# Kernel optimization log

Hardware: AMD Instinct MI355X
Metric: run time of the kernel (lower is better)

## Reference

```python
import jax, jax.numpy as jnp
import numpy as np
from jax import lax


def extract_patches(x, kh, kw, sh, sw):
    # x: [B,H,W,C] -> [B,oh,ow,kh,kw,C], same element order as tf.image.extract_patches
    B, H, W, C = x.shape
    oh = (H - kh) // sh + 1
    ow = (W - kw) // sw + 1
    rows = jnp.arange(oh)[:, None] * sh + jnp.arange(kh)[None, :]  # [oh,kh]
    cols = jnp.arange(ow)[:, None] * sw + jnp.arange(kw)[None, :]  # [ow,kw]
    p = x[:, rows]            # [B,oh,kh,W,C]
    p = p[:, :, :, cols]      # [B,oh,kh,ow,kw,C]
    return jnp.transpose(p, (0, 1, 3, 2, 4, 5))  # [B,oh,ow,kh,kw,C]


def fastgrnn(x, W, U, bg, bu, zeta, nu):
    # FastGRNN: z=sigmoid(Wx+Uh+bg); c=tanh(Wx+Uh+bu); h'=z*h+(sig(zeta)*(1-z)+sig(nu))*c
    # x: [N,T,D] -> final hidden [N,H]
    wx = jnp.einsum('ntd,dh->nth', x, W)  # precompute input projection
    z_gate = jax.nn.sigmoid(zeta)
    n_gate = jax.nn.sigmoid(nu)

    def step(h, wx_t):
        pre = wx_t + h @ U
        z = jax.nn.sigmoid(pre + bg)
        c = jnp.tanh(pre + bu)
        h_new = z * h + (z_gate * (1.0 - z) + n_gate) * c
        return h_new, None

    h0 = jnp.zeros((x.shape[0], W.shape[1]), x.dtype)
    hT, _ = lax.scan(step, h0, jnp.swapaxes(wx, 0, 1))  # scan over T
    return hT


def rnnpool_forward(inputs, W1, U1, bg1, bu1, zeta1, nu1,
                    W2, U2, bg2, bu2, zeta2, nu2, kh, kw, sh, sw):
    B, H, Wd, C = inputs.shape
    oh = (H - kh) // sh + 1
    ow = (Wd - kw) // sw + 1
    patches = extract_patches(inputs, kh, kw, sh, sw)          # [B,oh,ow,kh,kw,C]
    N = B * oh * ow
    p = patches.reshape(N, kh, kw, C)

    u = W1.shape[1]
    # row-wise: rnn1 scans along cols within each row
    x = p.reshape(N * kh, kw, C)
    h = fastgrnn(x, W1, U1, bg1, bu1, zeta1, nu1).reshape(N, kh, u)
    o21 = fastgrnn(h, W2, U2, bg2, bu2, zeta2, nu2)
    o22 = fastgrnn(h[:, ::-1, :], W2, U2, bg2, bu2, zeta2, nu2)

    # col-wise: transpose patch, rnn1 scans along rows within each col
    xc = jnp.transpose(p, (0, 2, 1, 3)).reshape(N * kw, kh, C)
    hc = fastgrnn(xc, W1, U1, bg1, bu1, zeta1, nu1).reshape(N, kw, u)
    o23 = fastgrnn(hc, W2, U2, bg2, bu2, zeta2, nu2)
    o24 = fastgrnn(hc[:, ::-1, :], W2, U2, bg2, bu2, zeta2, nu2)

    out = jnp.concatenate([o21, o22, o23, o24], axis=1)        # [N, 4*hOut]
    return out.reshape(B, oh, ow, -1)


def setup_inputs() -> dict:
    key = jax.random.key(0)
    ks = jax.random.split(key, 9)
    C, u, hout = 16, 8, 16  # in-channels, rnn1 hidden, rnn2 hidden (out_channel//4)
    s = 0.1
    inp = {
        'inputs': jax.random.normal(ks[0], (32, 112, 112, C), jnp.float32),
        'W1': jax.random.normal(ks[1], (C, u), jnp.float32) * s,
        'U1': jax.random.normal(ks[2], (u, u), jnp.float32) * s,
        'bg1': jnp.ones((u,), jnp.float32),
        'bu1': jnp.ones((u,), jnp.float32),
        'zeta1': jnp.float32(100.0),
        'nu1': jnp.float32(-100.0),
        'W2': jax.random.normal(ks[3], (u, hout), jnp.float32) * s,
        'U2': jax.random.normal(ks[4], (hout, hout), jnp.float32) * s,
        'bg2': jnp.ones((hout,), jnp.float32),
        'bu2': jnp.ones((hout,), jnp.float32),
        'zeta2': jnp.float32(100.0),
        'nu2': jnp.float32(-100.0),
        'kh': 8, 'kw': 8, 'sh': 4, 'sw': 4,
    }
    return inp


def reference(inputs, W1, U1, bg1, bu1, zeta1, nu1,
              W2, U2, bg2, bu2, zeta2, nu2, kh, kw, sh, sw):
    return rnnpool_forward(inputs, W1, U1, bg1, bu1, zeta1, nu1,
                           W2, U2, bg2, bu2, zeta2, nu2, kh, kw, sh, sw)
```

## Files before the change

kernel.cpp:

```cpp
#include <hip/hip_runtime.h>

#define PPB 4

typedef float v2f __attribute__((ext_vector_type(2)));

__device__ __forceinline__ float frcp(float x) { return __builtin_amdgcn_rcpf(x); }

__device__ __forceinline__ v2f vfma2(v2f a, v2f b, v2f c) {
#if __has_builtin(__builtin_amdgcn_pk_fma_f32)
  return __builtin_amdgcn_pk_fma_f32(a, b, c);
#elif __has_builtin(__builtin_elementwise_fma)
  return __builtin_elementwise_fma(a, b, c);
#else
  v2f d; d.x = fmaf(a.x, b.x, c.x); d.y = fmaf(a.y, b.y, c.y); return d;
#endif
}
__device__ __forceinline__ v2f vmul2(v2f a, v2f b) {
#if __has_builtin(__builtin_amdgcn_pk_mul_f32)
  return __builtin_amdgcn_pk_mul_f32(a, b);
#else
  return a * b;
#endif
}
__device__ __forceinline__ v2f vadd2(v2f a, v2f b) {
#if __has_builtin(__builtin_amdgcn_pk_add_f32)
  return __builtin_amdgcn_pk_add_f32(a, b);
#else
  return a + b;
#endif
}
__device__ __forceinline__ v2f bc(float x) { v2f p; p.x = x; p.y = x; return p; }

__device__ __forceinline__ v2f gate2(v2f pre, v2f h, v2f bgB, v2f KB, v2f nzgB,
                                     v2f AB, bool first) {
  v2f a = vadd2(pre, bgB);
  v2f s; s.x = __expf(-a.x); s.y = __expf(-a.y);
  v2f one = bc(1.f);
  v2f zd = vadd2(s, one);
  v2f z; z.x = frcp(zd.x); z.y = frcp(zd.y);
  v2f u = vmul2(vmul2(s, s), KB);
  v2f cd = vadd2(u, one);
  v2f cr; cr.x = frcp(cd.x); cr.y = frcp(cd.y);
  v2f cc = vfma2(cr, bc(2.f), bc(-1.f));
  v2f m = vfma2(z, nzgB, AB);
  v2f mc = vmul2(m, cc);
  return first ? mc : vfma2(z, h, mc);
}

__global__ __launch_bounds__(256) void l1_kernel(
    const float* __restrict__ inp, const float* __restrict__ W1,
    const float* __restrict__ U1, const float* __restrict__ bg1,
    const float* __restrict__ bu1, const float* __restrict__ zeta1,
    const float* __restrict__ nu1, float* __restrict__ hrowg,
    float* __restrict__ hcolg) {
  constexpr int NP = 6048;
  constexpr int SAs = 68;
  constexpr int SH = 18;

  __shared__ float w1s[128];
  __shared__ float wxs[PPB][16 * SAs];
  __shared__ v2f hp[PPB][7 * SH + 8];

  const int tid = threadIdx.x, wv = tid >> 6, lane = tid & 63;
  const int widx = blockIdx.x * PPB + wv;

  if (tid < 32) ((float4*)w1s)[tid] = ((const float4*)W1)[tid];
  __syncthreads();

  const bool isrow = widx < NP;
  const int v = isrow ? widx : widx - NP;
  const int b = v / 189;
  const int rem = v % 189;
  const int k = rem / 27;
  const int t27 = rem % 27;

  const int rr = lane >> 3, cc = lane & 7;
  const int ay = isrow ? (k * 16 + rr) : (t27 * 4 + rr);
  const int ax = isrow ? (t27 * 4 + cc) : (k * 16 + cc);
  const int by = isrow ? (ay + 8) : ay;
  const int bx = isrow ? ax : (ax + 8);

  {
    const float* pA = inp + ((size_t)(b * 112 + ay) * 112 + ax) * 16;
    const float* pB = inp + ((size_t)(b * 112 + by) * 112 + bx) * 16;
    float4 A0 = ((const float4*)pA)[0], A1 = ((const float4*)pA)[1],
           A2 = ((const float4*)pA)[2], A3 = ((const float4*)pA)[3];
    float4 B0 = ((const float4*)pB)[0], B1 = ((const float4*)pB)[1],
           B2 = ((const float4*)pB)[2], B3 = ((const float4*)pB)[3];
    float xA[16] = {A0.x, A0.y, A0.z, A0.w, A1.x, A1.y, A1.z, A1.w,
                    A2.x, A2.y, A2.z, A2.w, A3.x, A3.y, A3.z, A3.w};
    float xB[16] = {B0.x, B0.y, B0.z, B0.w, B1.x, B1.y, B1.z, B1.w,
                    B2.x, B2.y, B2.z, B2.w, B3.x, B3.y, B3.z, B3.w};
    v2f aA0 = bc(0.f), aA1 = bc(0.f), aA2 = bc(0.f), aA3 = bc(0.f);
    v2f aB0 = bc(0.f), aB1 = bc(0.f), aB2 = bc(0.f), aB3 = bc(0.f);
#pragma unroll
    for (int ci = 0; ci < 16; ++ci) {
      const v2f* wr = (const v2f*)&w1s[ci * 8];
      v2f w0 = wr[0], w1 = wr[1], w2 = wr[2], w3 = wr[3];
      v2f xa = bc(xA[ci]), xb = bc(xB[ci]);
      aA0 = vfma2(xa, w0, aA0); aA1 = vfma2(xa, w1, aA1);
      aA2 = vfma2(xa, w2, aA2); aA3 = vfma2(xa, w3, aA3);
      aB0 = vfma2(xb, w0, aB0); aB1 = vfma2(xb, w1, aB1);
      aB2 = vfma2(xb, w2, aB2); aB3 = vfma2(xb, w3, aB3);
    }
    const int a0 = isrow ? rr : cc;
    const int b0 = isrow ? cc : rr;
    float* wdA = &wxs[wv][a0 * SAs + b0 * 8];
    float* wdB = &wxs[wv][(a0 + 8) * SAs + b0 * 8];
    ((float4*)wdA)[0] = float4{aA0.x, aA0.y, aA1.x, aA1.y};
    ((float4*)wdA)[1] = float4{aA2.x, aA2.y, aA3.x, aA3.y};
    ((float4*)wdB)[0] = float4{aB0.x, aB0.y, aB1.x, aB1.y};
    ((float4*)wdB)[1] = float4{aB2.x, aB2.y, aB3.x, aB3.y};
  }
  __builtin_amdgcn_wave_barrier();

  const int seq = rr, hid = cc;
  v2f u1b[8];
#pragma unroll
  for (int i = 0; i < 8; ++i) u1b[i] = bc(U1[i * 8 + hid]);
  const float bg1v = bg1[hid], bu1v = bu1[hid];
  const float zg1 = frcp(1.f + __expf(-zeta1[0]));
  const float ng1 = frcp(1.f + __expf(-nu1[0]));
  const v2f bgB = bc(bg1v);
  const v2f KB = bc(__expf(2.f * (bg1v - bu1v)));
  const v2f nzgB = bc(-zg1);
  const v2f AB = bc(zg1 + ng1);

  v2f* hq = &hp[wv][0];
  v2f h = bc(0.f);
  {
    v2f pre;
    pre.x = wxs[wv][seq * SAs + hid];
    pre.y = wxs[wv][(seq + 8) * SAs + hid];
    h = gate2(pre, h, bgB, KB, nzgB, AB, true);
    hq[seq * SH + hid] = h;
  }
  __builtin_amdgcn_wave_barrier();
#pragma unroll
  for (int t = 1; t < 8; ++t) {
    const float4* hr4 = (const float4*)&hq[seq * SH];
    float4 f0 = hr4[0], f1 = hr4[1], f2 = hr4[2], f3 = hr4[3];
    v2f q = vmul2(v2f{f0.x, f0.y}, u1b[0]);
    q = vfma2(v2f{f0.z, f0.w}, u1b[1], q);
    q = vfma2(v2f{f1.x, f1.y}, u1b[2], q);
    q = vfma2(v2f{f1.z, f1.w}, u1b[3], q);
    q = vfma2(v2f{f2.x, f2.y}, u1b[4], q);
    q = vfma2(v2f{f2.z, f2.w}, u1b[5], q);
    q = vfma2(v2f{f3.x, f3.y}, u1b[6], q);
    q = vfma2(v2f{f3.z, f3.w}, u1b[7], q);
    v2f pre;
    pre.x = wxs[wv][seq * SAs + t * 8 + hid];
    pre.y = wxs[wv][(seq + 8) * SAs + t * 8 + hid];
    pre = vadd2(pre, q);
    h = gate2(pre, h, bgB, KB, nzgB, AB, false);
    hq[seq * SH + hid] = h;
    __builtin_amdgcn_wave_barrier();
  }

  const size_t obase = (((size_t)(b * 27 + t27) * 112) + k * 16 + seq) * 8 + hid;
  float* dst = isrow ? hrowg : hcolg;
  dst[obase] = h.x;
  dst[obase + 64] = h.y;
}

__global__ __launch_bounds__(256) void l2_kernel(
    const float* __restrict__ hrowg, const float* __restrict__ hcolg,
    const float* __restrict__ W2, const float* __restrict__ U2,
    const float* __restrict__ bg2, const float* __restrict__ bu2,
    const float* __restrict__ zeta2, const float* __restrict__ nu2,
    float* __restrict__ out) {
  constexpr int GST = 18;
  constexpr int WHT = 18;
  __shared__ v2f hbI[PPB][128];
  __shared__ v2f whb[PPB][2 * 8 * WHT];
  __shared__ v2f h2I[PPB][3 * GST + 16];

  const int tid = threadIdx.x, wv = tid >> 6, lane = tid & 63;
  const int w = blockIdx.x * PPB + wv;
  const int n0 = 2 * w, n1 = n0 + 1;

  {
    const int p = lane >> 5, half = (lane >> 4) & 1, idx = lane & 15;
    const int pn = p ? n1 : n0;
    const int pw = pn % 27;
    const int qq = pn / 27;
    const int ph = qq % 27, bb = qq / 27;
    const float* src = half ? &hcolg[(((size_t)(bb * 27 + ph)) * 112 + pw * 4) * 8]
                            : &hrowg[(((size_t)(bb * 27 + pw)) * 112 + ph * 4) * 8];
    float4 val = ((const float4*)src)[idx];
    float* base = (float*)&hbI[wv][half * 64 + idx * 4];
    base[0 + p] = val.x;
    base[2 + p] = val.y;
    base[4 + p] = val.z;
    base[6 + p] = val.w;
  }
  __builtin_amdgcn_wave_barrier();

  const int g = lane >> 4, j = lane & 15;
  v2f w2b[8], u2b[16];
#pragma unroll
  for (int d = 0; d < 8; ++d) w2b[d] = bc(W2[d * 16 + j]);
#pragma unroll
  for (int i = 0; i < 16; ++i) u2b[i] = bc(U2[i * 16 + j]);
  const float bg2v = bg2[j], bu2v = bu2[j];
  const float zg2 = frcp(1.f + __expf(-zeta2[0]));
  const float ng2 = frcp(1.f + __expf(-nu2[0]));
  const v2f bgB = bc(bg2v);
  const v2f KB = bc(__expf(2.f * (bg2v - bu2v)));
  const v2f nzgB = bc(-zg2);
  const v2f AB = bc(zg2 + ng2);

  const int src = g >> 1;

  {
    const v2f* hb = &hbI[wv][src * 64];
    const int t0 = (g & 1) * 4;
#pragma unroll
    for (int i = 0; i < 4; ++i) {
      const int t = t0 + i;
      const v2f* hr = &hb[t * 8];
      v2f p = vmul2(hr[0], w2b[0]);
#pragma unroll
      for (int d = 1; d < 8; ++d) p = vfma2(hr[d], w2b[d], p);
      whb[wv][(src * 8 + t) * WHT + j] = p;
    }
  }
  __builtin_amdgcn_wave_barrier();

  const v2f* whsrc = &whb[wv][src * 8 * WHT];
  v2f* h2q = &h2I[wv][g * GST];

  v2f h2 = bc(0.f);
  {
    const int tt = (g & 1) ? 7 : 0;
    v2f p = whsrc[tt * WHT + j];
    h2 = gate2(p, h2, bgB, KB, nzgB, AB, true);
    h2q[j] = h2;
  }
  __builtin_amdgcn_wave_barrier();
#pragma unroll
  for (int t = 1; t < 8; ++t) {
    const int tt = (g & 1) ? (7 - t) : t;
    v2f p = whsrc[tt * WHT + j];
    const float4* q4 = (const float4*)h2q;
    float4 v0 = q4[0], v1 = q4[1], v2_ = q4[2], v3 = q4[3];
    float4 v4 = q4[4], v5 = q4[5], v6 = q4[6], v7 = q4[7];
    v2f q = vmul2(v2f{v0.x, v0.y}, u2b[0]);
    q = vfma2(v2f{v0.z, v0.w}, u2b[1], q);
    q = vfma2(v2f{v1.x, v1.y}, u2b[2], q);
    q = vfma2(v2f{v1.z, v1.w}, u2b[3], q);
    q = vfma2(v2f{v2_.x, v2_.y}, u2b[4], q);
    q = vfma2(v2f{v2_.z, v2_.w}, u2b[5], q);
    q = vfma2(v2f{v3.x, v3.y}, u2b[6], q);
    q = vfma2(v2f{v3.z, v3.w}, u2b[7], q);
    q = vfma2(v2f{v4.x, v4.y}, u2b[8], q);
    q = vfma2(v2f{v4.z, v4.w}, u2b[9], q);
    q = vfma2(v2f{v5.x, v5.y}, u2b[10], q);
    q = vfma2(v2f{v5.z, v5.w}, u2b[11], q);
    q = vfma2(v2f{v6.x, v6.y}, u2b[12], q);
    q = vfma2(v2f{v6.z, v6.w}, u2b[13], q);
    q = vfma2(v2f{v7.x, v7.y}, u2b[14], q);
    q = vfma2(v2f{v7.z, v7.w}, u2b[15], q);
    v2f pre = vadd2(p, q);
    h2 = gate2(pre, h2, bgB, KB, nzgB, AB, false);
    if (t < 7) {
      h2q[j] = h2;
      __builtin_amdgcn_wave_barrier();
    }
  }

  out[(size_t)n0 * 64 + lane] = h2.x;
  out[(size_t)n1 * 64 + lane] = h2.y;
}

extern "C" void kernel_launch(void* const* d_in, const int* in_sizes, int n_in,
                              void* d_out, int out_size, void* d_ws, size_t ws_size,
                              hipStream_t stream) {
  const float* inp   = (const float*)d_in[0];
  const float* W1    = (const float*)d_in[1];
  const float* U1    = (const float*)d_in[2];
  const float* bg1   = (const float*)d_in[3];
  const float* bu1   = (const float*)d_in[4];
  const float* zeta1 = (const float*)d_in[5];
  const float* nu1   = (const float*)d_in[6];
  const float* W2    = (const float*)d_in[7];
  const float* U2    = (const float*)d_in[8];
  const float* bg2   = (const float*)d_in[9];
  const float* bu2   = (const float*)d_in[10];
  const float* zeta2 = (const float*)d_in[11];
  const float* nu2   = (const float*)d_in[12];
  float* out = (float*)d_out;

  const size_t HSZ = (size_t)32 * 27 * 112 * 8;
  float* hrowg = (float*)d_ws;
  float* hcolg = hrowg + HSZ;

  l1_kernel<<<dim3(3024), dim3(256), 0, stream>>>(
      inp, W1, U1, bg1, bu1, zeta1, nu1, hrowg, hcolg);
  l2_kernel<<<dim3(2916), dim3(256), 0, stream>>>(
      hrowg, hcolg, W2, U2, bg2, bu2, zeta2, nu2, out);
}
```

Before: 37.36 us.

## Restructure layer-1 RNN to share input projections across overlapping patches

The first-layer kernel now has each block cover a strip of two adjacent patch columns (or rows) across all 112 image rows. It computes the W1 input projection once per pixel into shared memory and reuses it for the overlapping patches, where before each patch recomputed it. Each thread then runs one full 8-step recurrence with the hidden state and U1 held in registers, removing the per-step shared-memory exchange and wave barriers. The trade-offs are fewer, larger blocks with only 112–224 of 256 threads active in the recurrence, a large shared tile, and dropping the explicit packed-FP32 builtins in favour of plain vector ops.

```diff
diff --git a/kernel.cpp b/kernel.cpp
--- a/kernel.cpp
+++ b/kernel.cpp
@@ -7,28 +7,14 @@
 __device__ __forceinline__ float frcp(float x) { return __builtin_amdgcn_rcpf(x); }
 
 __device__ __forceinline__ v2f vfma2(v2f a, v2f b, v2f c) {
-#if __has_builtin(__builtin_amdgcn_pk_fma_f32)
-  return __builtin_amdgcn_pk_fma_f32(a, b, c);
-#elif __has_builtin(__builtin_elementwise_fma)
+#if __has_builtin(__builtin_elementwise_fma)
   return __builtin_elementwise_fma(a, b, c);
 #else
   v2f d; d.x = fmaf(a.x, b.x, c.x); d.y = fmaf(a.y, b.y, c.y); return d;
 #endif
 }
-__device__ __forceinline__ v2f vmul2(v2f a, v2f b) {
-#if __has_builtin(__builtin_amdgcn_pk_mul_f32)
-  return __builtin_amdgcn_pk_mul_f32(a, b);
-#else
-  return a * b;
-#endif
-}
-__device__ __forceinline__ v2f vadd2(v2f a, v2f b) {
-#if __has_builtin(__builtin_amdgcn_pk_add_f32)
-  return __builtin_amdgcn_pk_add_f32(a, b);
-#else
-  return a + b;
-#endif
-}
+__device__ __forceinline__ v2f vmul2(v2f a, v2f b) { return a * b; }
+__device__ __forceinline__ v2f vadd2(v2f a, v2f b) { return a + b; }
 __device__ __forceinline__ v2f bc(float x) { v2f p; p.x = x; p.y = x; return p; }
 
 __device__ __forceinline__ v2f gate2(v2f pre, v2f h, v2f bgB, v2f KB, v2f nzgB,
@@ -47,120 +33,132 @@
   return first ? mc : vfma2(z, h, mc);
 }
 
-__global__ __launch_bounds__(256) void l1_kernel(
+__global__ __launch_bounds__(256, 4) void l1_kernel(
     const float* __restrict__ inp, const float* __restrict__ W1,
     const float* __restrict__ U1, const float* __restrict__ bg1,
     const float* __restrict__ bu1, const float* __restrict__ zeta1,
     const float* __restrict__ nu1, float* __restrict__ hrowg,
     float* __restrict__ hcolg) {
-  constexpr int NP = 6048;
-  constexpr int SAs = 68;
-  constexpr int SH = 18;
+  constexpr int ST = 98;
 
   __shared__ float w1s[128];
-  __shared__ float wxs[PPB][16 * SAs];
-  __shared__ v2f hp[PPB][7 * SH + 8];
-
-  const int tid = threadIdx.x, wv = tid >> 6, lane = tid & 63;
-  const int widx = blockIdx.x * PPB + wv;
+  __shared__ float wxs[112 * ST];
+
+  const int tid = threadIdx.x;
+  const int bid = blockIdx.x;
+  const bool isrow = bid < 448;
+  const int v = isrow ? bid : bid - 448;
+  const int b = v / 14, wp = v % 14;
+  const int base4 = 8 * wp;
+  const int span = (wp == 13) ? 8 : 12;
 
   if (tid < 32) ((float4*)w1s)[tid] = ((const float4*)W1)[tid];
   __syncthreads();
 
-  const bool isrow = widx < NP;
-  const int v = isrow ? widx : widx - NP;
-  const int b = v / 189;
-  const int rem = v % 189;
-  const int k = rem / 27;
-  const int t27 = rem % 27;
-
-  const int rr = lane >> 3, cc = lane & 7;
-  const int ay = isrow ? (k * 16 + rr) : (t27 * 4 + rr);
-  const int ax = isrow ? (t27 * 4 + cc) : (k * 16 + cc);
-  const int by = isrow ? (ay + 8) : ay;
-  const int bx = isrow ? ax : (ax + 8);
-
-  {
-    const float* pA = inp + ((size_t)(b * 112 + ay) * 112 + ax) * 16;
-    const float* pB = inp + ((size_t)(b * 112 + by) * 112 + bx) * 16;
-    float4 A0 = ((const float4*)pA)[0], A1 = ((const float4*)pA)[1],
-           A2 = ((const float4*)pA)[2], A3 = ((const float4*)pA)[3];
-    float4 B0 = ((const float4*)pB)[0], B1 = ((const float4*)pB)[1],
-           B2 = ((const float4*)pB)[2], B3 = ((const float4*)pB)[3];
-    float xA[16] = {A0.x, A0.y, A0.z, A0.w, A1.x, A1.y, A1.z, A1.w,
-                    A2.x, A2.y, A2.z, A2.w, A3.x, A3.y, A3.z, A3.w};
-    float xB[16] = {B0.x, B0.y, B0.z, B0.w, B1.x, B1.y, B1.z, B1.w,
-                    B2.x, B2.y, B2.z, B2.w, B3.x, B3.y, B3.z, B3.w};
-    v2f aA0 = bc(0.f), aA1 = bc(0.f), aA2 = bc(0.f), aA3 = bc(0.f);
-    v2f aB0 = bc(0.f), aB1 = bc(0.f), aB2 = bc(0.f), aB3 = bc(0.f);
-#pragma unroll
-    for (int ci = 0; ci < 16; ++ci) {
-      const v2f* wr = (const v2f*)&w1s[ci * 8];
-      v2f w0 = wr[0], w1 = wr[1], w2 = wr[2], w3 = wr[3];
-      v2f xa = bc(xA[ci]), xb = bc(xB[ci]);
-      aA0 = vfma2(xa, w0, aA0); aA1 = vfma2(xa, w1, aA1);
-      aA2 = vfma2(xa, w2, aA2); aA3 = vfma2(xa, w3, aA3);
-      aB0 = vfma2(xb, w0, aB0); aB1 = vfma2(xb, w1, aB1);
-      aB2 = vfma2(xb, w2, aB2); aB3 = vfma2(xb, w3, aB3);
-    }
-    const int a0 = isrow ? rr : cc;
-    const int b0 = isrow ? cc : rr;
-    float* wdA = &wxs[wv][a0 * SAs + b0 * 8];
-    float* wdB = &wxs[wv][(a0 + 8) * SAs + b0 * 8];
-    ((float4*)wdA)[0] = float4{aA0.x, aA0.y, aA1.x, aA1.y};
-    ((float4*)wdA)[1] = float4{aA2.x, aA2.y, aA3.x, aA3.y};
-    ((float4*)wdB)[0] = float4{aB0.x, aB0.y, aB1.x, aB1.y};
-    ((float4*)wdB)[1] = float4{aB2.x, aB2.y, aB3.x, aB3.y};
-  }
-  __builtin_amdgcn_wave_barrier();
-
-  const int seq = rr, hid = cc;
-  v2f u1b[8];
-#pragma unroll
-  for (int i = 0; i < 8; ++i) u1b[i] = bc(U1[i * 8 + hid]);
-  const float bg1v = bg1[hid], bu1v = bu1[hid];
-  const float zg1 = frcp(1.f + __expf(-zeta1[0]));
-  const float ng1 = frcp(1.f + __expf(-nu1[0]));
-  const v2f bgB = bc(bg1v);
-  const v2f KB = bc(__expf(2.f * (bg1v - bu1v)));
-  const v2f nzgB = bc(-zg1);
-  const v2f AB = bc(zg1 + ng1);
-
-  v2f* hq = &hp[wv][0];
-  v2f h = bc(0.f);
-  {
-    v2f pre;
-    pre.x = wxs[wv][seq * SAs + hid];
-    pre.y = wxs[wv][(seq + 8) * SAs + hid];
-    h = gate2(pre, h, bgB, KB, nzgB, AB, true);
-    hq[seq * SH + hid] = h;
-  }
-  __builtin_amdgcn_wave_barrier();
-#pragma unroll
-  for (int t = 1; t < 8; ++t) {
-    const float4* hr4 = (const float4*)&hq[seq * SH];
-    float4 f0 = hr4[0], f1 = hr4[1], f2 = hr4[2], f3 = hr4[3];
-    v2f q = vmul2(v2f{f0.x, f0.y}, u1b[0]);
-    q = vfma2(v2f{f0.z, f0.w}, u1b[1], q);
-    q = vfma2(v2f{f1.x, f1.y}, u1b[2], q);
-    q = vfma2(v2f{f1.z, f1.w}, u1b[3], q);
-    q = vfma2(v2f{f2.x, f2.y}, u1b[4], q);
-    q = vfma2(v2f{f2.z, f2.w}, u1b[5], q);
-    q = vfma2(v2f{f3.x, f3.y}, u1b[6], q);
-    q = vfma2(v2f{f3.z, f3.w}, u1b[7], q);
-    v2f pre;
-    pre.x = wxs[wv][seq * SAs + t * 8 + hid];
-    pre.y = wxs[wv][(seq + 8) * SAs + t * 8 + hid];
-    pre = vadd2(pre, q);
-    h = gate2(pre, h, bgB, KB, nzgB, AB, false);
-    hq[seq * SH + hid] = h;
-    __builtin_amdgcn_wave_barrier();
-  }
-
-  const size_t obase = (((size_t)(b * 27 + t27) * 112) + k * 16 + seq) * 8 + hid;
-  float* dst = isrow ? hrowg : hcolg;
-  dst[obase] = h.x;
-  dst[obase + 64] = h.y;
+  for (int p = tid; p < 1344; p += 256) {
+    int q, s;
+    if (isrow) { q = p / 12;  s = p % 12; }
+    else       { q = p % 112; s = p / 112; }
+    if (s < span) {
+      const float* px = isrow
+          ? inp + ((size_t)(b * 112 + q) * 112 + base4 + s) * 16
+          : inp + ((size_t)(b * 112 + base4 + s) * 112 + q) * 16;
+      float4 x0 = ((const float4*)px)[0], x1 = ((const float4*)px)[1],
+             x2 = ((const float4*)px)[2], x3 = ((const float4*)px)[3];
+      float xr[16] = {x0.x, x0.y, x0.z, x0.w, x1.x, x1.y, x1.z, x1.w,
+                      x2.x, x2.y, x2.z, x2.w, x3.x, x3.y, x3.z, x3.w};
+      float a0 = 0.f, a1 = 0.f, a2 = 0.f, a3 = 0.f,
+            a4 = 0.f, a5 = 0.f, a6 = 0.f, a7 = 0.f;
+#pragma unroll
+      for (int ci = 0; ci < 16; ++ci) {
+        float4 wL = *(const float4*)&w1s[ci * 8];
+        float4 wH = *(const float4*)&w1s[ci * 8 + 4];
+        a0 = fmaf(xr[ci], wL.x, a0); a1 = fmaf(xr[ci], wL.y, a1);
+        a2 = fmaf(xr[ci], wL.z, a2); a3 = fmaf(xr[ci], wL.w, a3);
+        a4 = fmaf(xr[ci], wH.x, a4); a5 = fmaf(xr[ci], wH.y, a5);
+        a6 = fmaf(xr[ci], wH.z, a6); a7 = fmaf(xr[ci], wH.w, a7);
+      }
+      float* wd = &wxs[q * ST + s * 8];
+      ((float2*)wd)[0] = float2{a0, a1};
+      ((float2*)wd)[1] = float2{a2, a3};
+      ((float2*)wd)[2] = float2{a4, a5};
+      ((float2*)wd)[3] = float2{a6, a7};
+    }
+  }
+
+  float u1r[8][8];
+#pragma unroll
+  for (int i = 0; i < 8; i += 2) {
+    float4 r0 = ((const float4*)U1)[i * 2 + 0];
+    float4 r1 = ((const float4*)U1)[i * 2 + 1];
+    float4 r2 = ((const float4*)U1)[i * 2 + 2];
+    float4 r3 = ((const float4*)U1)[i * 2 + 3];
+    u1r[i][0] = r0.x; u1r[i][1] = r0.y; u1r[i][2] = r0.z; u1r[i][3] = r0.w;
+    u1r[i][4] = r1.x; u1r[i][5] = r1.y; u1r[i][6] = r1.z; u1r[i][7] = r1.w;
+    u1r[i+1][0] = r2.x; u1r[i+1][1] = r2.y; u1r[i+1][2] = r2.z; u1r[i+1][3] = r2.w;
+    u1r[i+1][4] = r3.x; u1r[i+1][5] = r3.y; u1r[i+1][6] = r3.z; u1r[i+1][7] = r3.w;
+  }
+  float bgv[8], Kc[8];
+#pragma unroll
+  for (int j = 0; j < 8; ++j) {
+    bgv[j] = bg1[j];
+    Kc[j] = __expf(2.f * (bg1[j] - bu1[j]));
+  }
+  const float zg = frcp(1.f + __expf(-zeta1[0]));
+  const float ng = frcp(1.f + __expf(-nu1[0]));
+  const float A = zg + ng;
+
+  __syncthreads();
+
+  const int nact = (wp == 13) ? 112 : 224;
+  if (tid < nact) {
+    const int wl = tid / 112, r = tid % 112;
+    const int base = r * ST + wl * 32;
+    float h[8];
+    {
+      const float* w0p = &wxs[base];
+#pragma unroll
+      for (int j = 0; j < 8; ++j) {
+        float s = __expf(-(w0p[j] + bgv[j]));
+        float z = frcp(1.f + s);
+        float u = s * s * Kc[j];
+        float c = fmaf(2.f, frcp(1.f + u), -1.f);
+        float m = fmaf(-zg, z, A);
+        h[j] = m * c;
+      }
+    }
+#pragma unroll
+    for (int t = 1; t < 8; ++t) {
+      const float* wtp = &wxs[base + t * 8];
+      float qa[8];
+#pragma unroll
+      for (int j = 0; j < 8; ++j) {
+        float q = u1r[0][j] * h[0];
+        q = fmaf(u1r[1][j], h[1], q);
+        q = fmaf(u1r[2][j], h[2], q);
+        q = fmaf(u1r[3][j], h[3], q);
+        q = fmaf(u1r[4][j], h[4], q);
+        q = fmaf(u1r[5][j], h[5], q);
+        q = fmaf(u1r[6][j], h[6], q);
+        q = fmaf(u1r[7][j], h[7], q);
+        qa[j] = q;
+      }
+#pragma unroll
+      for (int j = 0; j < 8; ++j) {
+        float pre = wtp[j] + qa[j];
+        float s = __expf(-(pre + bgv[j]));
+        float z = frcp(1.f + s);
+        float u = s * s * Kc[j];
+        float c = fmaf(2.f, frcp(1.f + u), -1.f);
+        float m = fmaf(-zg, z, A);
+        h[j] = fmaf(z, h[j], m * c);
+      }
+    }
+    float* dst = (isrow ? hrowg : hcolg) +
+                 ((size_t)(b * 27 + 2 * wp + wl) * 112 + r) * 8;
+    ((float4*)dst)[0] = float4{h[0], h[1], h[2], h[3]};
+    ((float4*)dst)[1] = float4{h[4], h[5], h[6], h[7]};
+  }
 }
 
 __global__ __launch_bounds__(256) void l2_kernel(
@@ -295,7 +293,7 @@
   float* hrowg = (float*)d_ws;
   float* hcolg = hrowg + HSZ;
 
-  l1_kernel<<<dim3(3024), dim3(256), 0, stream>>>(
+  l1_kernel<<<dim3(896), dim3(256), 0, stream>>>(
       inp, W1, U1, bg1, bu1, zeta1, nu1, hrowg, hcolg);
   l2_kernel<<<dim3(2916), dim3(256), 0, stream>>>(
       hrowg, hcolg, W2, U2, bg2, bu2, zeta2, nu2, out);
```

Result: slower. 43.51 us (+16.5%).

## Precompute input projection once per pixel in separate kernel, store row and column layouts

Applied to the files above, without the earlier changes.

Adds a wx_kernel that computes the W1 input projection once per pixel and writes it in both row-major and transposed (column) layouts. l1_kernel then reads these precomputed projections from global memory instead of reloading 16-channel inputs and recomputing the projection for each overlapping patch. This removes redundant projection work and input reads caused by patch overlap (each pixel sits in several patches, both row and column passes). In exchange it adds a kernel launch, about 25 MB of extra global writes plus scattered transposed stores, and replaces the packed-math builtins with generic vector operators.

```diff
diff --git a/kernel.cpp b/kernel.cpp
--- a/kernel.cpp
+++ b/kernel.cpp
@@ -7,65 +7,84 @@
 __device__ __forceinline__ float frcp(float x) { return __builtin_amdgcn_rcpf(x); }
 
 __device__ __forceinline__ v2f vfma2(v2f a, v2f b, v2f c) {
-#if __has_builtin(__builtin_amdgcn_pk_fma_f32)
-  return __builtin_amdgcn_pk_fma_f32(a, b, c);
-#elif __has_builtin(__builtin_elementwise_fma)
+#if __has_builtin(__builtin_elementwise_fma)
   return __builtin_elementwise_fma(a, b, c);
 #else
   v2f d; d.x = fmaf(a.x, b.x, c.x); d.y = fmaf(a.y, b.y, c.y); return d;
 #endif
 }
-__device__ __forceinline__ v2f vmul2(v2f a, v2f b) {
-#if __has_builtin(__builtin_amdgcn_pk_mul_f32)
-  return __builtin_amdgcn_pk_mul_f32(a, b);
-#else
-  return a * b;
-#endif
-}
-__device__ __forceinline__ v2f vadd2(v2f a, v2f b) {
-#if __has_builtin(__builtin_amdgcn_pk_add_f32)
-  return __builtin_amdgcn_pk_add_f32(a, b);
-#else
-  return a + b;
-#endif
-}
 __device__ __forceinline__ v2f bc(float x) { v2f p; p.x = x; p.y = x; return p; }
 
 __device__ __forceinline__ v2f gate2(v2f pre, v2f h, v2f bgB, v2f KB, v2f nzgB,
                                      v2f AB, bool first) {
-  v2f a = vadd2(pre, bgB);
+  v2f a = pre + bgB;
   v2f s; s.x = __expf(-a.x); s.y = __expf(-a.y);
   v2f one = bc(1.f);
-  v2f zd = vadd2(s, one);
+  v2f zd = s + one;
   v2f z; z.x = frcp(zd.x); z.y = frcp(zd.y);
-  v2f u = vmul2(vmul2(s, s), KB);
-  v2f cd = vadd2(u, one);
+  v2f u = (s * s) * KB;
+  v2f cd = u + one;
   v2f cr; cr.x = frcp(cd.x); cr.y = frcp(cd.y);
   v2f cc = vfma2(cr, bc(2.f), bc(-1.f));
   v2f m = vfma2(z, nzgB, AB);
-  v2f mc = vmul2(m, cc);
+  v2f mc = m * cc;
   return first ? mc : vfma2(z, h, mc);
 }
 
+__global__ __launch_bounds__(256) void wx_kernel(
+    const float* __restrict__ inp, const float* __restrict__ W1,
+    float* __restrict__ wxr, float* __restrict__ wxc) {
+  const int tid = threadIdx.x, wv = tid >> 6, lane = tid & 63;
+  const int p = lane >> 3, j = lane & 7;
+  const int gw = blockIdx.x * 4 + wv;
+
+  float w1c[16];
+#pragma unroll
+  for (int ci = 0; ci < 16; ++ci) w1c[ci] = W1[ci * 8 + j];
+
+#pragma unroll 1
+  for (int it = 0; it < 16; ++it) {
+    const int pixel = (gw * 16 + it) * 8 + p;
+    const float* src = inp + (size_t)pixel * 16;
+    float4 x0 = ((const float4*)src)[0], x1 = ((const float4*)src)[1],
+           x2 = ((const float4*)src)[2], x3 = ((const float4*)src)[3];
+    float a = x0.x * w1c[0];
+    a = fmaf(x0.y, w1c[1], a);
+    a = fmaf(x0.z, w1c[2], a);
+    a = fmaf(x0.w, w1c[3], a);
+    a = fmaf(x1.x, w1c[4], a);
+    a = fmaf(x1.y, w1c[5], a);
+    a = fmaf(x1.z, w1c[6], a);
+    a = fmaf(x1.w, w1c[7], a);
+    a = fmaf(x2.x, w1c[8], a);
+    a = fmaf(x2.y, w1c[9], a);
+    a = fmaf(x2.z, w1c[10], a);
+    a = fmaf(x2.w, w1c[11], a);
+    a = fmaf(x3.x, w1c[12], a);
+    a = fmaf(x3.y, w1c[13], a);
+    a = fmaf(x3.z, w1c[14], a);
+    a = fmaf(x3.w, w1c[15], a);
+    wxr[(size_t)pixel * 8 + j] = a;
+    const int b = pixel / 12544;
+    const int rem = pixel - b * 12544;
+    const int y = rem / 112, x = rem - y * 112;
+    wxc[((size_t)(b * 112 + x) * 112 + y) * 8 + j] = a;
+  }
+}
+
 __global__ __launch_bounds__(256) void l1_kernel(
-    const float* __restrict__ inp, const float* __restrict__ W1,
+    const float* __restrict__ wxr, const float* __restrict__ wxc,
     const float* __restrict__ U1, const float* __restrict__ bg1,
     const float* __restrict__ bu1, const float* __restrict__ zeta1,
     const float* __restrict__ nu1, float* __restrict__ hrowg,
     float* __restrict__ hcolg) {
   constexpr int NP = 6048;
-  constexpr int SAs = 68;
   constexpr int SH = 18;
 
-  __shared__ float w1s[128];
-  __shared__ float wxs[PPB][16 * SAs];
   __shared__ v2f hp[PPB][7 * SH + 8];
 
   const int tid = threadIdx.x, wv = tid >> 6, lane = tid & 63;
   const int widx = blockIdx.x * PPB + wv;
-
-  if (tid < 32) ((float4*)w1s)[tid] = ((const float4*)W1)[tid];
-  __syncthreads();
 
   const bool isrow = widx < NP;
   const int v = isrow ? widx : widx - NP;
@@ -74,47 +93,12 @@
   const int k = rem / 27;
   const int t27 = rem % 27;
 
-  const int rr = lane >> 3, cc = lane & 7;
-  const int ay = isrow ? (k * 16 + rr) : (t27 * 4 + rr);
-  const int ax = isrow ? (t27 * 4 + cc) : (k * 16 + cc);
-  const int by = isrow ? (ay + 8) : ay;
-  const int bx = isrow ? ax : (ax + 8);
-
-  {
-    const float* pA = inp + ((size_t)(b * 112 + ay) * 112 + ax) * 16;
-    const float* pB = inp + ((size_t)(b * 112 + by) * 112 + bx) * 16;
-    float4 A0 = ((const float4*)pA)[0], A1 = ((const float4*)pA)[1],
-           A2 = ((const float4*)pA)[2], A3 = ((const float4*)pA)[3];
-    float4 B0 = ((const float4*)pB)[0], B1 = ((const float4*)pB)[1],
-           B2 = ((const float4*)pB)[2], B3 = ((const float4*)pB)[3];
-    float xA[16] = {A0.x, A0.y, A0.z, A0.w, A1.x, A1.y, A1.z, A1.w,
-                    A2.x, A2.y, A2.z, A2.w, A3.x, A3.y, A3.z, A3.w};
-    float xB[16] = {B0.x, B0.y, B0.z, B0.w, B1.x, B1.y, B1.z, B1.w,
-                    B2.x, B2.y, B2.z, B2.w, B3.x, B3.y, B3.z, B3.w};
-    v2f aA0 = bc(0.f), aA1 = bc(0.f), aA2 = bc(0.f), aA3 = bc(0.f);
-    v2f aB0 = bc(0.f), aB1 = bc(0.f), aB2 = bc(0.f), aB3 = bc(0.f);
-#pragma unroll
-    for (int ci = 0; ci < 16; ++ci) {
-      const v2f* wr = (const v2f*)&w1s[ci * 8];
-      v2f w0 = wr[0], w1 = wr[1], w2 = wr[2], w3 = wr[3];
-      v2f xa = bc(xA[ci]), xb = bc(xB[ci]);
-      aA0 = vfma2(xa, w0, aA0); aA1 = vfma2(xa, w1, aA1);
-      aA2 = vfma2(xa, w2, aA2); aA3 = vfma2(xa, w3, aA3);
-      aB0 = vfma2(xb, w0, aB0); aB1 = vfma2(xb, w1, aB1);
-      aB2 = vfma2(xb, w2, aB2); aB3 = vfma2(xb, w3, aB3);
-    }
-    const int a0 = isrow ? rr : cc;
-    const int b0 = isrow ? cc : rr;
-    float* wdA = &wxs[wv][a0 * SAs + b0 * 8];
-    float* wdB = &wxs[wv][(a0 + 8) * SAs + b0 * 8];
-    ((float4*)wdA)[0] = float4{aA0.x, aA0.y, aA1.x, aA1.y};
-    ((float4*)wdA)[1] = float4{aA2.x, aA2.y, aA3.x, aA3.y};
-    ((float4*)wdB)[0] = float4{aB0.x, aB0.y, aB1.x, aB1.y};
-    ((float4*)wdB)[1] = float4{aB2.x, aB2.y, aB3.x, aB3.y};
-  }
-  __builtin_amdgcn_wave_barrier();
-
-  const int seq = rr, hid = cc;
+  const int seq = lane >> 3, hid = lane & 7;
+
+  const float* wxbase = isrow ? wxr : wxc;
+  const size_t base0 = ((size_t)(b * 112 + k * 16 + seq) * 112 + t27 * 4) * 8 + hid;
+  const size_t base1 = base0 + (size_t)8 * 112 * 8;
+
   v2f u1b[8];
 #pragma unroll
   for (int i = 0; i < 8; ++i) u1b[i] = bc(U1[i * 8 + hid]);
@@ -130,8 +114,8 @@
   v2f h = bc(0.f);
   {
     v2f pre;
-    pre.x = wxs[wv][seq * SAs + hid];
-    pre.y = wxs[wv][(seq + 8) * SAs + hid];
+    pre.x = wxbase[base0];
+    pre.y = wxbase[base1];
     h = gate2(pre, h, bgB, KB, nzgB, AB, true);
     hq[seq * SH + hid] = h;
   }
@@ -140,7 +124,7 @@
   for (int t = 1; t < 8; ++t) {
     const float4* hr4 = (const float4*)&hq[seq * SH];
     float4 f0 = hr4[0], f1 = hr4[1], f2 = hr4[2], f3 = hr4[3];
-    v2f q = vmul2(v2f{f0.x, f0.y}, u1b[0]);
+    v2f q = v2f{f0.x, f0.y} * u1b[0];
     q = vfma2(v2f{f0.z, f0.w}, u1b[1], q);
     q = vfma2(v2f{f1.x, f1.y}, u1b[2], q);
     q = vfma2(v2f{f1.z, f1.w}, u1b[3], q);
@@ -149,9 +133,9 @@
     q = vfma2(v2f{f3.x, f3.y}, u1b[6], q);
     q = vfma2(v2f{f3.z, f3.w}, u1b[7], q);
     v2f pre;
-    pre.x = wxs[wv][seq * SAs + t * 8 + hid];
-    pre.y = wxs[wv][(seq + 8) * SAs + t * 8 + hid];
-    pre = vadd2(pre, q);
+    pre.x = wxbase[base0 + t * 8];
+    pre.y = wxbase[base1 + t * 8];
+    pre = pre + q;
     h = gate2(pre, h, bgB, KB, nzgB, AB, false);
     hq[seq * SH + hid] = h;
     __builtin_amdgcn_wave_barrier();
@@ -219,7 +203,7 @@
     for (int i = 0; i < 4; ++i) {
       const int t = t0 + i;
       const v2f* hr = &hb[t * 8];
-      v2f p = vmul2(hr[0], w2b[0]);
+      v2f p = hr[0] * w2b[0];
 #pragma unroll
       for (int d = 1; d < 8; ++d) p = vfma2(hr[d], w2b[d], p);
       whb[wv][(src * 8 + t) * WHT + j] = p;
@@ -245,7 +229,7 @@
     const float4* q4 = (const float4*)h2q;
     float4 v0 = q4[0], v1 = q4[1], v2_ = q4[2], v3 = q4[3];
     float4 v4 = q4[4], v5 = q4[5], v6 = q4[6], v7 = q4[7];
-    v2f q = vmul2(v2f{v0.x, v0.y}, u2b[0]);
+    v2f q = v2f{v0.x, v0.y} * u2b[0];
     q = vfma2(v2f{v0.z, v0.w}, u2b[1], q);
     q = vfma2(v2f{v1.x, v1.y}, u2b[2], q);
     q = vfma2(v2f{v1.z, v1.w}, u2b[3], q);
@@ -261,7 +245,7 @@
     q = vfma2(v2f{v6.z, v6.w}, u2b[13], q);
     q = vfma2(v2f{v7.x, v7.y}, u2b[14], q);
     q = vfma2(v2f{v7.z, v7.w}, u2b[15], q);
-    v2f pre = vadd2(p, q);
+    v2f pre = p + q;
     h2 = gate2(pre, h2, bgB, KB, nzgB, AB, false);
     if (t < 7) {
       h2q[j] = h2;
@@ -291,12 +275,16 @@
   const float* nu2   = (const float*)d_in[12];
   float* out = (float*)d_out;
 
+  const size_t WXSZ = (size_t)32 * 112 * 112 * 8;
   const size_t HSZ = (size_t)32 * 27 * 112 * 8;
-  float* hrowg = (float*)d_ws;
+  float* wxr = (float*)d_ws;
+  float* wxc = wxr + WXSZ;
+  float* hrowg = wxc + WXSZ;
   float* hcolg = hrowg + HSZ;
 
+  wx_kernel<<<dim3(784), dim3(256), 0, stream>>>(inp, W1, wxr, wxc);
   l1_kernel<<<dim3(3024), dim3(256), 0, stream>>>(
-      inp, W1, U1, bg1, bu1, zeta1, nu1, hrowg, hcolg);
+      wxr, wxc, U1, bg1, bu1, zeta1, nu1, hrowg, hcolg);
   l2_kernel<<<dim3(2916), dim3(256), 0, stream>>>(
       hrowg, hcolg, W2, U2, bg2, bu2, zeta2, nu2, out);
 }
```

After: 49.64 us, median of 2. 1.33x slower.
